# Kernel tuning notes

Hardware: AMD Instinct MI355X
Metric: run time of the kernel (lower is better)

Reference implementation:

```python
import jax, jax.numpy as jnp
import numpy as np

EMB = 128
N_LEFT = 100000
N_RIGHT = 100000
N_EDGES = 600000
EDGE_FEAT = 1


def _ortho(key, shape):
    a = jax.random.normal(key, shape, dtype=jnp.float32)
    q, r = jnp.linalg.qr(a if shape[0] >= shape[1] else a.T)
    q = q * jnp.sign(jnp.diag(r))
    return q if shape[0] >= shape[1] else q.T


def setup_inputs() -> dict:
    key = jax.random.key(0)
    ks = jax.random.split(key, 12)
    return {
        "left_features": jax.random.normal(ks[0], (N_LEFT, EMB), dtype=jnp.float32),
        "edge_indices": jax.random.randint(ks[1], (2, N_EDGES), 0, N_LEFT, dtype=jnp.int32).astype(jnp.int64),
        "edge_features": jax.random.normal(ks[2], (N_EDGES, EDGE_FEAT), dtype=jnp.float32),
        "right_features": jax.random.normal(ks[3], (N_RIGHT, EMB), dtype=jnp.float32),
        "scatter_out_size": N_RIGHT,
        # parameters (orthogonal weights, zero biases, unit PreNorm scales)
        "W_left": _ortho(ks[4], (EMB, EMB)),
        "b_left": jnp.zeros((EMB,), jnp.float32),
        "W_edge": _ortho(ks[5], (EMB, EDGE_FEAT)),
        "W_right": _ortho(ks[6], (EMB, EMB)),
        "scale_final": jnp.ones((1,), jnp.float32),
        "W_final": _ortho(ks[7], (EMB, EMB)),
        "b_final": jnp.zeros((EMB,), jnp.float32),
        "scale_post": jnp.ones((1,), jnp.float32),
        "W_out1": _ortho(ks[8], (EMB, 2 * EMB)),
        "b_out1": jnp.zeros((EMB,), jnp.float32),
        "W_out2": _ortho(ks[9], (EMB, EMB)),
        "b_out2": jnp.zeros((EMB,), jnp.float32),
    }


def reference(left_features, edge_indices, edge_features, right_features,
              scatter_out_size, W_left, b_left, W_edge, W_right,
              scale_final, W_final, b_final, scale_post,
              W_out1, b_out1, W_out2, b_out2):
    # node / edge projections
    left_proj = left_features @ W_left.T + b_left            # [n_left, emb]
    edge_proj = edge_features @ W_edge.T                     # [n_edges, emb]
    right_proj = right_features @ W_right.T                  # [n_right, emb]
    # gather per-edge messages and combine
    joint = left_proj[edge_indices[0]] + edge_proj + right_proj[edge_indices[1]]
    # feature_module_final: PreNorm(scale only) -> ReLU -> Linear
    joint = jax.nn.relu(joint * scale_final) @ W_final.T + b_final
    # scatter-add onto right-side nodes (right_to_left=False)
    conv = jax.ops.segment_sum(joint, edge_indices[1], num_segments=scatter_out_size)
    conv = conv * scale_post
    # output MLP on [conv ; prev_right]
    h = jnp.concatenate([conv, right_features], axis=1)      # [n_right, 2*emb]
    h = jax.nn.relu(h @ W_out1.T + b_out1)
    return h @ W_out2.T + b_out2
```

## Files before the change

### kernel.cpp

```cpp
#include <hip/hip_runtime.h>

#define EMB 128

typedef __attribute__((ext_vector_type(8))) short short8;
typedef __attribute__((ext_vector_type(4))) float floatx4;

#define MFMA(a, b, c) __builtin_amdgcn_mfma_f32_16x16x32_bf16((a), (b), (c), 0, 0, 0)

__device__ __forceinline__ ushort f2b(float f) {
    unsigned u = __float_as_uint(f);
    return (ushort)((u + 0x7fff + ((u >> 16) & 1)) >> 16);
}
__device__ __forceinline__ float b2f(ushort h) {
    return __uint_as_float(((unsigned)h) << 16);
}
__device__ __forceinline__ short8 cvt8(const float* p) {
    float4 f0 = *(const float4*)p;
    float4 f1 = *(const float4*)(p + 4);
    short8 v;
    v[0] = f2b(f0.x); v[1] = f2b(f0.y); v[2] = f2b(f0.z); v[3] = f2b(f0.w);
    v[4] = f2b(f1.x); v[5] = f2b(f1.y); v[6] = f2b(f1.z); v[7] = f2b(f1.w);
    return v;
}

__global__ __launch_bounds__(256) void k_cvthist(const float* __restrict__ w0,
                                                 const float* __restrict__ w1,
                                                 const float* __restrict__ w2,
                                                 const float* __restrict__ w3,
                                                 const float* __restrict__ w4,
                                                 ushort* __restrict__ dst,
                                                 const int* __restrict__ eidx,
                                                 int* __restrict__ cnt,
                                                 int n_edges) {
    int bid = blockIdx.x;
    if (bid < 384) {
        int i = bid * 256 + threadIdx.x;
        const float* src; int off;
        if (i < 16384)      { src = w0; off = i; }
        else if (i < 32768) { src = w1; off = i - 16384; }
        else if (i < 49152) { src = w2; off = i - 32768; }
        else if (i < 81920) { src = w3; off = i - 49152; }
        else                { src = w4; off = i - 81920; }
        dst[i] = f2b(src[off]);
    } else {
        int e = (bid - 384) * 256 + threadIdx.x;
        if (e < n_edges) atomicAdd(&cnt[eidx[n_edges + e]], 1);
    }
}

#define SCAN_CHUNK 4096
__global__ __launch_bounds__(1024) void k_scan1(const int* __restrict__ cnt,
                                                int* __restrict__ offs,
                                                int* __restrict__ bsum, int n) {
    __shared__ int buf[1024];
    int t = threadIdx.x;
    int i0 = blockIdx.x * SCAN_CHUNK + t * 4;
    int v[4];
#pragma unroll
    for (int u = 0; u < 4; u++) { int i = i0 + u; v[u] = (i < n) ? cnt[i] : 0; }
    int s = v[0] + v[1] + v[2] + v[3];
    buf[t] = s;
    __syncthreads();
    for (int d = 1; d < 1024; d <<= 1) {
        int x = (t >= d) ? buf[t - d] : 0;
        __syncthreads();
        buf[t] += x;
        __syncthreads();
    }
    int excl = buf[t] - s;
#pragma unroll
    for (int u = 0; u < 4; u++) { int i = i0 + u; if (i < n) offs[i] = excl; excl += v[u]; }
    if (t == 1023) bsum[blockIdx.x] = buf[1023];
}

__global__ __launch_bounds__(1024) void k_scan2(const int* __restrict__ bsum,
                                                int* __restrict__ offs,
                                                int* __restrict__ cursor, int n) {
    int bid = blockIdx.x;
    int base = 0;
    for (int j = 0; j < bid; j++) base += bsum[j];
    int i0 = bid * SCAN_CHUNK + threadIdx.x * 4;
#pragma unroll
    for (int u = 0; u < 4; u++) {
        int i = i0 + u;
        if (i < n) { int o = offs[i] + base; offs[i] = o; cursor[i] = o; }
    }
}

__global__ __launch_bounds__(256) void k_permproj(const int* __restrict__ eidx,
                                                  const float* __restrict__ ef,
                                                  int* __restrict__ cursor,
                                                  int2* __restrict__ sle,
                                                  int n_edges,
                                                  const float* __restrict__ XL,
                                                  const float* __restrict__ XR,
                                                  const ushort* __restrict__ WLb,
                                                  const ushort* __restrict__ WRb,
                                                  const float* __restrict__ bias,
                                                  ushort* __restrict__ YL,
                                                  ushort* __restrict__ YR,
                                                  int n, int eb, int nblk) {
    int bid = blockIdx.x;
    if (bid < eb) {
        int e = bid * 256 + threadIdx.x;
        if (e < n_edges) {
            int r = eidx[n_edges + e];
            int p = atomicAdd(&cursor[r], 1);
            int2 v; v.x = eidx[e]; v.y = __float_as_int(ef[e]);
            sle[p] = v;
        }
        return;
    }
    bid -= eb;
    const float* X; const ushort* Wb; ushort* Y; int has_bias;
    if (bid < nblk) { X = XL; Wb = WLb; Y = YL; has_bias = 1; }
    else            { X = XR; Wb = WRb; Y = YR; has_bias = 0; bid -= nblk; }

    int t = threadIdx.x, wave = t >> 6, lane = t & 63;
    int m = lane & 15, quad = lane >> 4;
    int rp = (wave & 1) * 32, colg = (wave >> 1) * 64;
    size_t row0 = (size_t)bid * 64;

    short8 a[2][4];
#pragma unroll
    for (int rt = 0; rt < 2; rt++) {
        size_t row = row0 + rp + rt * 16 + m;
        if (row > (size_t)(n - 1)) row = (size_t)(n - 1);
        const float* xr = X + row * EMB;
#pragma unroll
        for (int ks = 0; ks < 4; ks++)
            a[rt][ks] = cvt8(xr + ks * 32 + quad * 8);
    }
#pragma unroll
    for (int ct = 0; ct < 4; ct++) {
        int col = colg + ct * 16 + m;
        floatx4 acc0 = {0.f, 0.f, 0.f, 0.f}, acc1 = {0.f, 0.f, 0.f, 0.f};
#pragma unroll
        for (int ks = 0; ks < 4; ks++) {
            short8 b = *(const short8*)(Wb + (size_t)col * EMB + ks * 32 + quad * 8);
            acc0 = MFMA(a[0][ks], b, acc0);
            acc1 = MFMA(a[1][ks], b, acc1);
        }
        float bb = has_bias ? bias[col] : 0.f;
        size_t r0 = row0 + rp + quad * 4;
#pragma unroll
        for (int r = 0; r < 4; r++) {
            size_t row = r0 + r;
            if (row < (size_t)n) Y[row * EMB + col] = f2b(acc0[r] + bb);
            row += 16;
            if (row < (size_t)n) Y[row * EMB + col] = f2b(acc1[r] + bb);
        }
    }
}

__global__ __launch_bounds__(256) void k_reduce(const ushort* __restrict__ Pl,
                                                const ushort* __restrict__ Pr,
                                                const int2* __restrict__ sle,
                                                const float* __restrict__ We,
                                                const int* __restrict__ offs,
                                                const float* __restrict__ scale_final,
                                                ushort* __restrict__ S,
                                                int n_right, int n_edges) {
    int r = blockIdx.x * 4 + (threadIdx.x >> 6);
    int lane = threadIdx.x & 63;
    float scale = scale_final[0];
    float2 we = *(const float2*)(We + lane * 2);
    ushort2 pru = *(const ushort2*)(Pr + (size_t)r * EMB + lane * 2);
    float prx = b2f(pru.x), pry = b2f(pru.y);
    float ax = 0.f, ay = 0.f;
    int s0 = offs[r];
    int s1 = (r + 1 < n_right) ? offs[r + 1] : n_edges;
    int ei = s0;
    for (; ei + 4 <= s1; ei += 4) {
        int2 e0 = sle[ei], e1 = sle[ei + 1], e2 = sle[ei + 2], e3 = sle[ei + 3];
        ushort2 p0 = *(const ushort2*)(Pl + (size_t)e0.x * EMB + lane * 2);
        ushort2 p1 = *(const ushort2*)(Pl + (size_t)e1.x * EMB + lane * 2);
        ushort2 p2 = *(const ushort2*)(Pl + (size_t)e2.x * EMB + lane * 2);
        ushort2 p3 = *(const ushort2*)(Pl + (size_t)e3.x * EMB + lane * 2);
        float f0 = __int_as_float(e0.y), f1 = __int_as_float(e1.y);
        float f2_ = __int_as_float(e2.y), f3 = __int_as_float(e3.y);
        ax += fmaxf((b2f(p0.x) + prx + f0 * we.x) * scale, 0.f);
        ay += fmaxf((b2f(p0.y) + pry + f0 * we.y) * scale, 0.f);
        ax += fmaxf((b2f(p1.x) + prx + f1 * we.x) * scale, 0.f);
        ay += fmaxf((b2f(p1.y) + pry + f1 * we.y) * scale, 0.f);
        ax += fmaxf((b2f(p2.x) + prx + f2_ * we.x) * scale, 0.f);
        ay += fmaxf((b2f(p2.y) + pry + f2_ * we.y) * scale, 0.f);
        ax += fmaxf((b2f(p3.x) + prx + f3 * we.x) * scale, 0.f);
        ay += fmaxf((b2f(p3.y) + pry + f3 * we.y) * scale, 0.f);
    }
    for (; ei < s1; ei++) {
        int2 e0 = sle[ei];
        ushort2 p0 = *(const ushort2*)(Pl + (size_t)e0.x * EMB + lane * 2);
        float f0 = __int_as_float(e0.y);
        ax += fmaxf((b2f(p0.x) + prx + f0 * we.x) * scale, 0.f);
        ay += fmaxf((b2f(p0.y) + pry + f0 * we.y) * scale, 0.f);
    }
    ushort2 o; o.x = f2b(ax); o.y = f2b(ay);
    *(ushort2*)(S + (size_t)r * EMB + lane * 2) = o;
}

__global__ __launch_bounds__(256) void k_out_mfma(const ushort* __restrict__ S,
                                                  const float* __restrict__ right,
                                                  const ushort* __restrict__ Wfb,
                                                  const float* __restrict__ bf,
                                                  const int* __restrict__ deg,
                                                  const float* __restrict__ sc_post,
                                                  const ushort* __restrict__ W1b,
                                                  const float* __restrict__ b1,
                                                  const ushort* __restrict__ W2b,
                                                  const float* __restrict__ b2,
                                                  float* __restrict__ out, int n) {
    __shared__ ushort H[64][136];
    __shared__ float degs[64];
    int t = threadIdx.x, wave = t >> 6, lane = t & 63;
    int m = lane & 15, quad = lane >> 4;
    int rp = (wave & 1) * 32, colg = (wave >> 1) * 64;
    size_t row0 = (size_t)blockIdx.x * 64;
    float sp = sc_post[0];

    if (t < 64) {
        size_t rr = row0 + t;
        degs[t] = (rr < (size_t)n) ? (float)deg[rr] : 0.f;
    }

    short8 a1[2][4], ar[2][4];
#pragma unroll
    for (int rt = 0; rt < 2; rt++) {
        size_t row = row0 + rp + rt * 16 + m;
        if (row > (size_t)(n - 1)) row = (size_t)(n - 1);
        const ushort* sr = S + row * EMB;
        const float* rr = right + row * EMB;
#pragma unroll
        for (int ks = 0; ks < 4; ks++) {
            a1[rt][ks] = *(const short8*)(sr + ks * 32 + quad * 8);
            ar[rt][ks] = cvt8(rr + ks * 32 + quad * 8);
        }
    }
    __syncthreads();

#pragma unroll
    for (int ct = 0; ct < 4; ct++) {
        int col = colg + ct * 16 + m;
        floatx4 acc0 = {0.f, 0.f, 0.f, 0.f}, acc1 = {0.f, 0.f, 0.f, 0.f};
#pragma unroll
        for (int ks = 0; ks < 4; ks++) {
            short8 b = *(const short8*)(Wfb + (size_t)col * EMB + ks * 32 + quad * 8);
            acc0 = MFMA(a1[0][ks], b, acc0);
            acc1 = MFMA(a1[1][ks], b, acc1);
        }
        float bb = bf[col];
        int r0 = rp + quad * 4;
#pragma unroll
        for (int r = 0; r < 4; r++) {
            H[r0 + r][col]      = f2b((acc0[r] + degs[r0 + r] * bb) * sp);
            H[r0 + 16 + r][col] = f2b((acc1[r] + degs[r0 + 16 + r] * bb) * sp);
        }
    }
    __syncthreads();

    short8 a2[2][4];
#pragma unroll
    for (int rt = 0; rt < 2; rt++)
#pragma unroll
        for (int ks = 0; ks < 4; ks++)
            a2[rt][ks] = *(const short8*)(&H[rp + rt * 16 + m][ks * 32 + quad * 8]);
    __syncthreads();

#pragma unroll
    for (int ct = 0; ct < 4; ct++) {
        int col = colg + ct * 16 + m;
        floatx4 acc0 = {0.f, 0.f, 0.f, 0.f}, acc1 = {0.f, 0.f, 0.f, 0.f};
        const ushort* wrow = W1b + (size_t)col * 256;
#pragma unroll
        for (int ks = 0; ks < 4; ks++) {
            short8 b = *(const short8*)(wrow + ks * 32 + quad * 8);
            acc0 = MFMA(a2[0][ks], b, acc0);
            acc1 = MFMA(a2[1][ks], b, acc1);
        }
#pragma unroll
        for (int ks = 0; ks < 4; ks++) {
            short8 b = *(const short8*)(wrow + 128 + ks * 32 + quad * 8);
            acc0 = MFMA(ar[0][ks], b, acc0);
            acc1 = MFMA(ar[1][ks], b, acc1);
        }
        float bb = b1[col];
        int r0 = rp + quad * 4;
#pragma unroll
        for (int r = 0; r < 4; r++) {
            H[r0 + r][col]      = f2b(fmaxf(acc0[r] + bb, 0.f));
            H[r0 + 16 + r][col] = f2b(fmaxf(acc1[r] + bb, 0.f));
        }
    }
    __syncthreads();

    short8 a3[2][4];
#pragma unroll
    for (int rt = 0; rt < 2; rt++)
#pragma unroll
        for (int ks = 0; ks < 4; ks++)
            a3[rt][ks] = *(const short8*)(&H[rp + rt * 16 + m][ks * 32 + quad * 8]);
#pragma unroll
    for (int ct = 0; ct < 4; ct++) {
        int col = colg + ct * 16 + m;
        floatx4 acc0 = {0.f, 0.f, 0.f, 0.f}, acc1 = {0.f, 0.f, 0.f, 0.f};
#pragma unroll
        for (int ks = 0; ks < 4; ks++) {
            short8 b = *(const short8*)(W2b + (size_t)col * EMB + ks * 32 + quad * 8);
            acc0 = MFMA(a3[0][ks], b, acc0);
            acc1 = MFMA(a3[1][ks], b, acc1);
        }
        float bb = b2[col];
        size_t r0 = row0 + rp + quad * 4;
#pragma unroll
        for (int r = 0; r < 4; r++) {
            size_t row = r0 + r;
            if (row < (size_t)n) out[row * EMB + col] = acc0[r] + bb;
            row += 16;
            if (row < (size_t)n) out[row * EMB + col] = acc1[r] + bb;
        }
    }
}

extern "C" void kernel_launch(void* const* d_in, const int* in_sizes, int n_in,
                              void* d_out, int out_size, void* d_ws, size_t ws_size,
                              hipStream_t stream) {
    const float* left   = (const float*)d_in[0];
    const int*   eidx   = (const int*)  d_in[1];
    const float* efeat  = (const float*)d_in[2];
    const float* right  = (const float*)d_in[3];
    const float* W_left = (const float*)d_in[5];
    const float* b_left = (const float*)d_in[6];
    const float* W_edge = (const float*)d_in[7];
    const float* W_right= (const float*)d_in[8];
    const float* sc_fin = (const float*)d_in[9];
    const float* W_fin  = (const float*)d_in[10];
    const float* b_fin  = (const float*)d_in[11];
    const float* sc_post= (const float*)d_in[12];
    const float* W_out1 = (const float*)d_in[13];
    const float* b_out1 = (const float*)d_in[14];
    const float* W_out2 = (const float*)d_in[15];
    const float* b_out2 = (const float*)d_in[16];

    int n_left  = in_sizes[0] / EMB;
    int n_edges = in_sizes[2];
    int n_right = in_sizes[3] / EMB;

    ushort* us = (ushort*)d_ws;
    ushort* Wl_b = us;
    ushort* Wr_b = us + 16384;
    ushort* Wf_b = us + 32768;
    ushort* W1_b = us + 49152;
    ushort* W2_b = us + 81920;
    ushort* Pl   = us + 98304;
    ushort* Pr   = Pl + (size_t)n_left * EMB;
    ushort* S    = Pr + (size_t)n_right * EMB;
    int* cnt    = (int*)(S + (size_t)n_right * EMB);
    int* offs   = cnt + n_right;
    int* cursor = offs + n_right;
    int* bsum   = cursor + n_right;
    int2* sle   = (int2*)(bsum + 64);

    hipMemsetAsync(cnt, 0, (size_t)n_right * sizeof(int), stream);

    int eb = (n_edges + 255) / 256;
    int nblk = (n_left + 63) / 64;

    k_cvthist<<<384 + eb, 256, 0, stream>>>(W_left, W_right, W_fin, W_out1,
                                            W_out2, us, eidx, cnt, n_edges);

    int nsb = (n_right + SCAN_CHUNK - 1) / SCAN_CHUNK;
    k_scan1<<<nsb, 1024, 0, stream>>>(cnt, offs, bsum, n_right);
    k_scan2<<<nsb, 1024, 0, stream>>>(bsum, offs, cursor, n_right);

    k_permproj<<<eb + 2 * nblk, 256, 0, stream>>>(eidx, efeat, cursor, sle,
                                                  n_edges, left, right,
                                                  Wl_b, Wr_b, b_left,
                                                  Pl, Pr, n_left, eb, nblk);

    k_reduce<<<n_right / 4, 256, 0, stream>>>(Pl, Pr, sle, W_edge, offs,
                                              sc_fin, S, n_right, n_edges);

    k_out_mfma<<<(n_right + 63) / 64, 256, 0, stream>>>(S, right, Wf_b, b_fin,
                                                        cnt, sc_post, W1_b, b_out1,
                                                        W2_b, b_out2,
                                                        (float*)d_out, n_right);
}
```

Before: 405.2 us.

## Fuse edge reduction into output MLP kernel and transpose MFMA operand layout

Merges the per-right-node edge reduction with the three-layer output MLP into one kernel, so the aggregated rows stay in shared memory instead of round-tripping through a global bf16 buffer. Each wave now owns 16 rows and computes all 128 output columns by swapping MFMA operands (weights as A, activations as B), which lets each lane store four contiguous outputs as vector writes. The projection kernel gets the same restructuring. In exchange, each wave walks 16 rows serially in the reduction, so latency hiding rests on fewer concurrent gathers per wave, and weight reuse across row tiles within a wave is lost.

```diff
diff --git a/kernel.cpp b/kernel.cpp
--- a/kernel.cpp
+++ b/kernel.cpp
@@ -3,6 +3,7 @@
 #define EMB 128
 
 typedef __attribute__((ext_vector_type(8))) short short8;
+typedef __attribute__((ext_vector_type(4))) short short4v;
 typedef __attribute__((ext_vector_type(4))) float floatx4;
 
 #define MFMA(a, b, c) __builtin_amdgcn_mfma_f32_16x16x32_bf16((a), (b), (c), 0, 0, 0)
@@ -118,205 +119,186 @@
 
     int t = threadIdx.x, wave = t >> 6, lane = t & 63;
     int m = lane & 15, quad = lane >> 4;
-    int rp = (wave & 1) * 32, colg = (wave >> 1) * 64;
     size_t row0 = (size_t)bid * 64;
-
-    short8 a[2][4];
-#pragma unroll
-    for (int rt = 0; rt < 2; rt++) {
-        size_t row = row0 + rp + rt * 16 + m;
-        if (row > (size_t)(n - 1)) row = (size_t)(n - 1);
-        const float* xr = X + row * EMB;
-#pragma unroll
-        for (int ks = 0; ks < 4; ks++)
-            a[rt][ks] = cvt8(xr + ks * 32 + quad * 8);
-    }
-#pragma unroll
-    for (int ct = 0; ct < 4; ct++) {
-        int col = colg + ct * 16 + m;
-        floatx4 acc0 = {0.f, 0.f, 0.f, 0.f}, acc1 = {0.f, 0.f, 0.f, 0.f};
-#pragma unroll
-        for (int ks = 0; ks < 4; ks++) {
-            short8 b = *(const short8*)(Wb + (size_t)col * EMB + ks * 32 + quad * 8);
-            acc0 = MFMA(a[0][ks], b, acc0);
-            acc1 = MFMA(a[1][ks], b, acc1);
-        }
-        float bb = has_bias ? bias[col] : 0.f;
-        size_t r0 = row0 + rp + quad * 4;
-#pragma unroll
-        for (int r = 0; r < 4; r++) {
-            size_t row = r0 + r;
-            if (row < (size_t)n) Y[row * EMB + col] = f2b(acc0[r] + bb);
-            row += 16;
-            if (row < (size_t)n) Y[row * EMB + col] = f2b(acc1[r] + bb);
-        }
-    }
-}
-
-__global__ __launch_bounds__(256) void k_reduce(const ushort* __restrict__ Pl,
+    size_t row = row0 + wave * 16 + m;
+    size_t rowc = (row < (size_t)n) ? row : (size_t)(n - 1);
+
+    short8 xf[4];
+    const float* xr = X + rowc * EMB;
+#pragma unroll
+    for (int ks = 0; ks < 4; ks++)
+        xf[ks] = cvt8(xr + ks * 32 + quad * 8);
+
+    bool ok = (row < (size_t)n);
+#pragma unroll
+    for (int wt = 0; wt < 8; wt++) {
+        floatx4 acc = {0.f, 0.f, 0.f, 0.f};
+#pragma unroll
+        for (int ks = 0; ks < 4; ks++) {
+            short8 w = *(const short8*)(Wb + (size_t)(wt * 16 + m) * EMB + ks * 32 + quad * 8);
+            acc = MFMA(w, xf[ks], acc);
+        }
+        float b0 = 0.f, b1_ = 0.f, b2_ = 0.f, b3 = 0.f;
+        if (has_bias) {
+            float4 bb = *(const float4*)(bias + wt * 16 + quad * 4);
+            b0 = bb.x; b1_ = bb.y; b2_ = bb.z; b3 = bb.w;
+        }
+        if (ok) {
+            short4v o;
+            o[0] = f2b(acc[0] + b0);
+            o[1] = f2b(acc[1] + b1_);
+            o[2] = f2b(acc[2] + b2_);
+            o[3] = f2b(acc[3] + b3);
+            *(short4v*)(Y + row * EMB + wt * 16 + quad * 4) = o;
+        }
+    }
+}
+
+__global__ __launch_bounds__(256) void k_redout(const ushort* __restrict__ Pl,
                                                 const ushort* __restrict__ Pr,
                                                 const int2* __restrict__ sle,
                                                 const float* __restrict__ We,
                                                 const int* __restrict__ offs,
                                                 const float* __restrict__ scale_final,
-                                                ushort* __restrict__ S,
-                                                int n_right, int n_edges) {
-    int r = blockIdx.x * 4 + (threadIdx.x >> 6);
-    int lane = threadIdx.x & 63;
-    float scale = scale_final[0];
-    float2 we = *(const float2*)(We + lane * 2);
-    ushort2 pru = *(const ushort2*)(Pr + (size_t)r * EMB + lane * 2);
-    float prx = b2f(pru.x), pry = b2f(pru.y);
-    float ax = 0.f, ay = 0.f;
-    int s0 = offs[r];
-    int s1 = (r + 1 < n_right) ? offs[r + 1] : n_edges;
-    int ei = s0;
-    for (; ei + 4 <= s1; ei += 4) {
-        int2 e0 = sle[ei], e1 = sle[ei + 1], e2 = sle[ei + 2], e3 = sle[ei + 3];
-        ushort2 p0 = *(const ushort2*)(Pl + (size_t)e0.x * EMB + lane * 2);
-        ushort2 p1 = *(const ushort2*)(Pl + (size_t)e1.x * EMB + lane * 2);
-        ushort2 p2 = *(const ushort2*)(Pl + (size_t)e2.x * EMB + lane * 2);
-        ushort2 p3 = *(const ushort2*)(Pl + (size_t)e3.x * EMB + lane * 2);
-        float f0 = __int_as_float(e0.y), f1 = __int_as_float(e1.y);
-        float f2_ = __int_as_float(e2.y), f3 = __int_as_float(e3.y);
-        ax += fmaxf((b2f(p0.x) + prx + f0 * we.x) * scale, 0.f);
-        ay += fmaxf((b2f(p0.y) + pry + f0 * we.y) * scale, 0.f);
-        ax += fmaxf((b2f(p1.x) + prx + f1 * we.x) * scale, 0.f);
-        ay += fmaxf((b2f(p1.y) + pry + f1 * we.y) * scale, 0.f);
-        ax += fmaxf((b2f(p2.x) + prx + f2_ * we.x) * scale, 0.f);
-        ay += fmaxf((b2f(p2.y) + pry + f2_ * we.y) * scale, 0.f);
-        ax += fmaxf((b2f(p3.x) + prx + f3 * we.x) * scale, 0.f);
-        ay += fmaxf((b2f(p3.y) + pry + f3 * we.y) * scale, 0.f);
-    }
-    for (; ei < s1; ei++) {
-        int2 e0 = sle[ei];
-        ushort2 p0 = *(const ushort2*)(Pl + (size_t)e0.x * EMB + lane * 2);
-        float f0 = __int_as_float(e0.y);
-        ax += fmaxf((b2f(p0.x) + prx + f0 * we.x) * scale, 0.f);
-        ay += fmaxf((b2f(p0.y) + pry + f0 * we.y) * scale, 0.f);
-    }
-    ushort2 o; o.x = f2b(ax); o.y = f2b(ay);
-    *(ushort2*)(S + (size_t)r * EMB + lane * 2) = o;
-}
-
-__global__ __launch_bounds__(256) void k_out_mfma(const ushort* __restrict__ S,
-                                                  const float* __restrict__ right,
-                                                  const ushort* __restrict__ Wfb,
-                                                  const float* __restrict__ bf,
-                                                  const int* __restrict__ deg,
-                                                  const float* __restrict__ sc_post,
-                                                  const ushort* __restrict__ W1b,
-                                                  const float* __restrict__ b1,
-                                                  const ushort* __restrict__ W2b,
-                                                  const float* __restrict__ b2,
-                                                  float* __restrict__ out, int n) {
+                                                const float* __restrict__ right,
+                                                const ushort* __restrict__ Wfb,
+                                                const float* __restrict__ bf,
+                                                const float* __restrict__ sc_post,
+                                                const ushort* __restrict__ W1b,
+                                                const float* __restrict__ b1,
+                                                const ushort* __restrict__ W2b,
+                                                const float* __restrict__ b2,
+                                                float* __restrict__ out,
+                                                int n, int n_edges) {
     __shared__ ushort H[64][136];
     __shared__ float degs[64];
     int t = threadIdx.x, wave = t >> 6, lane = t & 63;
     int m = lane & 15, quad = lane >> 4;
-    int rp = (wave & 1) * 32, colg = (wave >> 1) * 64;
     size_t row0 = (size_t)blockIdx.x * 64;
+    float scale = scale_final[0];
     float sp = sc_post[0];
-
-    if (t < 64) {
-        size_t rr = row0 + t;
-        degs[t] = (rr < (size_t)n) ? (float)deg[rr] : 0.f;
-    }
-
-    short8 a1[2][4], ar[2][4];
-#pragma unroll
-    for (int rt = 0; rt < 2; rt++) {
-        size_t row = row0 + rp + rt * 16 + m;
-        if (row > (size_t)(n - 1)) row = (size_t)(n - 1);
-        const ushort* sr = S + row * EMB;
-        const float* rr = right + row * EMB;
-#pragma unroll
-        for (int ks = 0; ks < 4; ks++) {
-            a1[rt][ks] = *(const short8*)(sr + ks * 32 + quad * 8);
-            ar[rt][ks] = cvt8(rr + ks * 32 + quad * 8);
-        }
-    }
-    __syncthreads();
-
-#pragma unroll
-    for (int ct = 0; ct < 4; ct++) {
-        int col = colg + ct * 16 + m;
-        floatx4 acc0 = {0.f, 0.f, 0.f, 0.f}, acc1 = {0.f, 0.f, 0.f, 0.f};
-#pragma unroll
-        for (int ks = 0; ks < 4; ks++) {
-            short8 b = *(const short8*)(Wfb + (size_t)col * EMB + ks * 32 + quad * 8);
-            acc0 = MFMA(a1[0][ks], b, acc0);
-            acc1 = MFMA(a1[1][ks], b, acc1);
-        }
-        float bb = bf[col];
-        int r0 = rp + quad * 4;
-#pragma unroll
-        for (int r = 0; r < 4; r++) {
-            H[r0 + r][col]      = f2b((acc0[r] + degs[r0 + r] * bb) * sp);
-            H[r0 + 16 + r][col] = f2b((acc1[r] + degs[r0 + 16 + r] * bb) * sp);
-        }
-    }
-    __syncthreads();
-
-    short8 a2[2][4];
-#pragma unroll
-    for (int rt = 0; rt < 2; rt++)
-#pragma unroll
-        for (int ks = 0; ks < 4; ks++)
-            a2[rt][ks] = *(const short8*)(&H[rp + rt * 16 + m][ks * 32 + quad * 8]);
-    __syncthreads();
-
-#pragma unroll
-    for (int ct = 0; ct < 4; ct++) {
-        int col = colg + ct * 16 + m;
-        floatx4 acc0 = {0.f, 0.f, 0.f, 0.f}, acc1 = {0.f, 0.f, 0.f, 0.f};
-        const ushort* wrow = W1b + (size_t)col * 256;
-#pragma unroll
-        for (int ks = 0; ks < 4; ks++) {
-            short8 b = *(const short8*)(wrow + ks * 32 + quad * 8);
-            acc0 = MFMA(a2[0][ks], b, acc0);
-            acc1 = MFMA(a2[1][ks], b, acc1);
-        }
-#pragma unroll
-        for (int ks = 0; ks < 4; ks++) {
-            short8 b = *(const short8*)(wrow + 128 + ks * 32 + quad * 8);
-            acc0 = MFMA(ar[0][ks], b, acc0);
-            acc1 = MFMA(ar[1][ks], b, acc1);
-        }
-        float bb = b1[col];
-        int r0 = rp + quad * 4;
-#pragma unroll
-        for (int r = 0; r < 4; r++) {
-            H[r0 + r][col]      = f2b(fmaxf(acc0[r] + bb, 0.f));
-            H[r0 + 16 + r][col] = f2b(fmaxf(acc1[r] + bb, 0.f));
-        }
-    }
-    __syncthreads();
-
-    short8 a3[2][4];
-#pragma unroll
-    for (int rt = 0; rt < 2; rt++)
-#pragma unroll
-        for (int ks = 0; ks < 4; ks++)
-            a3[rt][ks] = *(const short8*)(&H[rp + rt * 16 + m][ks * 32 + quad * 8]);
-#pragma unroll
-    for (int ct = 0; ct < 4; ct++) {
-        int col = colg + ct * 16 + m;
-        floatx4 acc0 = {0.f, 0.f, 0.f, 0.f}, acc1 = {0.f, 0.f, 0.f, 0.f};
-#pragma unroll
-        for (int ks = 0; ks < 4; ks++) {
-            short8 b = *(const short8*)(W2b + (size_t)col * EMB + ks * 32 + quad * 8);
-            acc0 = MFMA(a3[0][ks], b, acc0);
-            acc1 = MFMA(a3[1][ks], b, acc1);
-        }
-        float bb = b2[col];
-        size_t r0 = row0 + rp + quad * 4;
-#pragma unroll
-        for (int r = 0; r < 4; r++) {
-            size_t row = r0 + r;
-            if (row < (size_t)n) out[row * EMB + col] = acc0[r] + bb;
-            row += 16;
-            if (row < (size_t)n) out[row * EMB + col] = acc1[r] + bb;
+    float2 we = *(const float2*)(We + lane * 2);
+
+    for (int i = 0; i < 16; i++) {
+        int rl = wave * 16 + i;
+        size_t r = row0 + rl;
+        float ax = 0.f, ay = 0.f;
+        int dg = 0;
+        if (r < (size_t)n) {
+            ushort2 pru = *(const ushort2*)(Pr + r * EMB + lane * 2);
+            float prx = b2f(pru.x), pry = b2f(pru.y);
+            int s0 = offs[r];
+            int s1 = (r + 1 < (size_t)n) ? offs[r + 1] : n_edges;
+            dg = s1 - s0;
+            int ei = s0;
+            for (; ei + 4 <= s1; ei += 4) {
+                int2 e0 = sle[ei], e1 = sle[ei + 1], e2 = sle[ei + 2], e3 = sle[ei + 3];
+                ushort2 p0 = *(const ushort2*)(Pl + (size_t)e0.x * EMB + lane * 2);
+                ushort2 p1 = *(const ushort2*)(Pl + (size_t)e1.x * EMB + lane * 2);
+                ushort2 p2 = *(const ushort2*)(Pl + (size_t)e2.x * EMB + lane * 2);
+                ushort2 p3 = *(const ushort2*)(Pl + (size_t)e3.x * EMB + lane * 2);
+                float f0 = __int_as_float(e0.y), f1 = __int_as_float(e1.y);
+                float f2_ = __int_as_float(e2.y), f3 = __int_as_float(e3.y);
+                ax += fmaxf((b2f(p0.x) + prx + f0 * we.x) * scale, 0.f);
+                ay += fmaxf((b2f(p0.y) + pry + f0 * we.y) * scale, 0.f);
+                ax += fmaxf((b2f(p1.x) + prx + f1 * we.x) * scale, 0.f);
+                ay += fmaxf((b2f(p1.y) + pry + f1 * we.y) * scale, 0.f);
+                ax += fmaxf((b2f(p2.x) + prx + f2_ * we.x) * scale, 0.f);
+                ay += fmaxf((b2f(p2.y) + pry + f2_ * we.y) * scale, 0.f);
+                ax += fmaxf((b2f(p3.x) + prx + f3 * we.x) * scale, 0.f);
+                ay += fmaxf((b2f(p3.y) + pry + f3 * we.y) * scale, 0.f);
+            }
+            for (; ei < s1; ei++) {
+                int2 e0 = sle[ei];
+                ushort2 p0 = *(const ushort2*)(Pl + (size_t)e0.x * EMB + lane * 2);
+                float f0 = __int_as_float(e0.y);
+                ax += fmaxf((b2f(p0.x) + prx + f0 * we.x) * scale, 0.f);
+                ay += fmaxf((b2f(p0.y) + pry + f0 * we.y) * scale, 0.f);
+            }
+        }
+        ushort2 o; o.x = f2b(ax); o.y = f2b(ay);
+        *(ushort2*)(&H[rl][lane * 2]) = o;
+        if (lane == 0) degs[rl] = (float)dg;
+    }
+
+    int rl = wave * 16 + m;
+    size_t xrow = row0 + rl;
+    size_t xrowc = (xrow < (size_t)n) ? xrow : (size_t)(n - 1);
+    bool ok = (xrow < (size_t)n);
+    float dd = degs[rl];
+
+    short8 s4[4], ar[4];
+    const float* rr = right + xrowc * EMB;
+#pragma unroll
+    for (int ks = 0; ks < 4; ks++) {
+        s4[ks] = *(const short8*)(&H[rl][ks * 32 + quad * 8]);
+        ar[ks] = cvt8(rr + ks * 32 + quad * 8);
+    }
+
+#pragma unroll
+    for (int wt = 0; wt < 8; wt++) {
+        floatx4 acc = {0.f, 0.f, 0.f, 0.f};
+#pragma unroll
+        for (int ks = 0; ks < 4; ks++) {
+            short8 w = *(const short8*)(Wfb + (size_t)(wt * 16 + m) * EMB + ks * 32 + quad * 8);
+            acc = MFMA(w, s4[ks], acc);
+        }
+        float4 bb = *(const float4*)(bf + wt * 16 + quad * 4);
+        short4v o;
+        o[0] = f2b((acc[0] + dd * bb.x) * sp);
+        o[1] = f2b((acc[1] + dd * bb.y) * sp);
+        o[2] = f2b((acc[2] + dd * bb.z) * sp);
+        o[3] = f2b((acc[3] + dd * bb.w) * sp);
+        *(short4v*)(&H[rl][wt * 16 + quad * 4]) = o;
+    }
+
+    short8 c4[4];
+#pragma unroll
+    for (int ks = 0; ks < 4; ks++)
+        c4[ks] = *(const short8*)(&H[rl][ks * 32 + quad * 8]);
+#pragma unroll
+    for (int wt = 0; wt < 8; wt++) {
+        floatx4 acc = {0.f, 0.f, 0.f, 0.f};
+        const ushort* wrow = W1b + (size_t)(wt * 16 + m) * 256;
+#pragma unroll
+        for (int ks = 0; ks < 4; ks++) {
+            short8 w = *(const short8*)(wrow + ks * 32 + quad * 8);
+            acc = MFMA(w, c4[ks], acc);
+        }
+#pragma unroll
+        for (int ks = 0; ks < 4; ks++) {
+            short8 w = *(const short8*)(wrow + 128 + ks * 32 + quad * 8);
+            acc = MFMA(w, ar[ks], acc);
+        }
+        float4 bb = *(const float4*)(b1 + wt * 16 + quad * 4);
+        short4v o;
+        o[0] = f2b(fmaxf(acc[0] + bb.x, 0.f));
+        o[1] = f2b(fmaxf(acc[1] + bb.y, 0.f));
+        o[2] = f2b(fmaxf(acc[2] + bb.z, 0.f));
+        o[3] = f2b(fmaxf(acc[3] + bb.w, 0.f));
+        *(short4v*)(&H[rl][wt * 16 + quad * 4]) = o;
+    }
+
+    short8 h4[4];
+#pragma unroll
+    for (int ks = 0; ks < 4; ks++)
+        h4[ks] = *(const short8*)(&H[rl][ks * 32 + quad * 8]);
+#pragma unroll
+    for (int wt = 0; wt < 8; wt++) {
+        floatx4 acc = {0.f, 0.f, 0.f, 0.f};
+#pragma unroll
+        for (int ks = 0; ks < 4; ks++) {
+            short8 w = *(const short8*)(W2b + (size_t)(wt * 16 + m) * EMB + ks * 32 + quad * 8);
+            acc = MFMA(w, h4[ks], acc);
+        }
+        if (ok) {
+            float4 bb = *(const float4*)(b2 + wt * 16 + quad * 4);
+            float4 o;
+            o.x = acc[0] + bb.x;
+            o.y = acc[1] + bb.y;
+            o.z = acc[2] + bb.z;
+            o.w = acc[3] + bb.w;
+            *(float4*)(out + xrow * EMB + wt * 16 + quad * 4) = o;
         }
     }
 }
@@ -377,11 +359,10 @@
                                                   Wl_b, Wr_b, b_left,
                                                   Pl, Pr, n_left, eb, nblk);
 
-    k_reduce<<<n_right / 4, 256, 0, stream>>>(Pl, Pr, sle, W_edge, offs,
-                                              sc_fin, S, n_right, n_edges);
-
-    k_out_mfma<<<(n_right + 63) / 64, 256, 0, stream>>>(S, right, Wf_b, b_fin,
-                                                        cnt, sc_post, W1_b, b_out1,
-                                                        W2_b, b_out2,
-                                                        (float*)d_out, n_right);
-}
+    k_redout<<<(n_right + 63) / 64, 256, 0, stream>>>(Pl, Pr, sle, W_edge, offs,
+                                                      sc_fin, right, Wf_b, b_fin,
+                                                      sc_post, W1_b, b_out1,
+                                                      W2_b, b_out2,
+                                                      (float*)d_out,
+                                                      n_right, n_edges);
+}
```

New measurement: 466.1 us. 1.15x slower.
